# Optimization experiments

Measured on AMD Instinct MI355X. Metric: run time of the kernel, lower is better.

## Reference

```python
import jax, jax.numpy as jnp
import numpy as np

OUT_FEATURES = 4096
IN_FEATURES = 16384
NNZ = 2_000_000
BATCH = 128


def setup_inputs() -> dict:
    key = jax.random.key(0)
    k1, k2, k3, k4, k5 = jax.random.split(key, 5)
    inputs = jax.random.normal(k1, (BATCH, IN_FEATURES), dtype=jnp.float32)
    # learned sparse weight values and bias (uniform init like reset_parameters)
    bound = 1.0 / (IN_FEATURES ** 0.5)
    values = jax.random.uniform(k2, (NNZ,), minval=-bound, maxval=bound, dtype=jnp.float32)
    bias = jax.random.uniform(k3, (OUT_FEATURES,), minval=-bound, maxval=bound, dtype=jnp.float32)
    # fixed COO connectivity: rows -> out_features, cols -> in_features
    rows = jax.random.randint(k4, (NNZ,), 0, OUT_FEATURES, dtype=jnp.int32)
    cols = jax.random.randint(k5, (NNZ,), 0, IN_FEATURES, dtype=jnp.int32)
    return {"inputs": inputs, "values": values, "bias": bias, "rows": rows, "cols": cols}


def reference(inputs, values, bias, rows, cols):
    # out[b, r] = sum_{k: rows[k]==r} values[k] * inputs[b, cols[k]]  (+ bias[r])
    # Gather input columns per nnz entry, scale, then scatter-add into output rows.
    contrib = inputs[:, cols] * values            # [B, nnz]
    out = jax.ops.segment_sum(contrib.T, rows, num_segments=OUT_FEATURES).T  # [B, out_features]
    return out + bias
```

## Files before the change

### kernel.cpp

```cpp
#include <hip/hip_runtime.h>
#include <hip/hip_fp16.h>

#define NNZ    2000000
#define BATCH  128
#define IN_F   16384
#define OUT_F  4096
#define NCH    512
#define CHUNK  ((NNZ + NCH - 1) / NCH)
#define NBK    512
#define RPB    8
#define BK_CAP 4352
#define SP_CAP 2608

__global__ __launch_bounds__(512)
void k_bhist(const int* __restrict__ rows, int* __restrict__ bcntT) {
  __shared__ int h[NBK];
  const int t = threadIdx.x, c = blockIdx.x;
  h[t] = 0;
  __syncthreads();
  const int base = c * CHUNK;
  const int n = min(CHUNK, NNZ - base);
  for (int i = t; i < n; i += 512) atomicAdd(&h[rows[base + i] >> 3], 1);
  __syncthreads();
  bcntT[t * NCH + c] = h[t];
}

__global__ __launch_bounds__(256)
void k_cscan(int* __restrict__ bcntT, int* __restrict__ totals) {
  const int w = threadIdx.x >> 6, lane = threadIdx.x & 63;
  const int b = blockIdx.x * 4 + w;
  int4 u = ((const int4*)(bcntT + b * NCH))[lane * 2];
  int4 v = ((const int4*)(bcntT + b * NCH))[lane * 2 + 1];
  int p0 = 0, p1 = u.x, p2 = p1 + u.y, p3 = p2 + u.z, p4 = p3 + u.w;
  int p5 = p4 + v.x, p6 = p5 + v.y, p7 = p6 + v.z;
  int run = p7 + v.w;
  int x = run;
#pragma unroll
  for (int off = 1; off < 64; off <<= 1) { int y = __shfl_up(x, off); if (lane >= off) x += y; }
  const int e0 = x - run;
  int4 o0 = make_int4(e0 + p0, e0 + p1, e0 + p2, e0 + p3);
  int4 o1 = make_int4(e0 + p4, e0 + p5, e0 + p6, e0 + p7);
  ((int4*)(bcntT + b * NCH))[lane * 2] = o0;
  ((int4*)(bcntT + b * NCH))[lane * 2 + 1] = o1;
  if (lane == 63) totals[b] = x;
}

__global__ __launch_bounds__(64)
void k_sscan(const int* __restrict__ totals, int* __restrict__ bstart) {
  const int lane = threadIdx.x;
  int4 u = ((const int4*)totals)[lane * 2];
  int4 v = ((const int4*)totals)[lane * 2 + 1];
  int p0 = 0, p1 = u.x, p2 = p1 + u.y, p3 = p2 + u.z, p4 = p3 + u.w;
  int p5 = p4 + v.x, p6 = p5 + v.y, p7 = p6 + v.z;
  int run = p7 + v.w;
  int x = run;
#pragma unroll
  for (int off = 1; off < 64; off <<= 1) { int y = __shfl_up(x, off); if (lane >= off) x += y; }
  const int e0 = x - run;
  ((int4*)bstart)[lane * 2] = make_int4(e0 + p0, e0 + p1, e0 + p2, e0 + p3);
  ((int4*)bstart)[lane * 2 + 1] = make_int4(e0 + p4, e0 + p5, e0 + p6, e0 + p7);
  if (lane == 63) bstart[NBK] = x;
}

__global__ __launch_bounds__(512)
void k_bscatter(const int* __restrict__ rows, const int* __restrict__ cols,
                const float* __restrict__ vals, const int* __restrict__ bcntT,
                const int* __restrict__ bstart, int2* __restrict__ pairs1) {
  __shared__ int2 stage[CHUNK];
  __shared__ int h[NBK], lst[NBK], cnt[NBK], gb[NBK];
  const int t = threadIdx.x, c = blockIdx.x;
  h[t] = 0;
  __syncthreads();
  const int base = c * CHUNK;
  const int n = min(CHUNK, NNZ - base);
  for (int i = t; i < n; i += 512) atomicAdd(&h[rows[base + i] >> 3], 1);
  __syncthreads();
  if (t < 64) {
    const int l8 = t * 8;
    int v[8], pre[8], run = 0;
#pragma unroll
    for (int j = 0; j < 8; ++j) v[j] = h[l8 + j];
#pragma unroll
    for (int j = 0; j < 8; ++j) { pre[j] = run; run += v[j]; }
    int x = run;
#pragma unroll
    for (int off = 1; off < 64; off <<= 1) { int y = __shfl_up(x, off); if (t >= off) x += y; }
    const int e0 = x - run;
#pragma unroll
    for (int j = 0; j < 8; ++j) {
      const int b = l8 + j;
      const int lv = e0 + pre[j];
      lst[b] = lv; cnt[b] = lv;
      gb[b] = bstart[b] + bcntT[b * NCH + c] - lv;
    }
  }
  __syncthreads();
  for (int i = t; i < n; i += 512) {
    const int r = rows[base + i];
    const int pos = atomicAdd(&cnt[r >> 3], 1);
    stage[pos] = make_int2((r << 14) | cols[base + i], __float_as_int(vals[base + i]));
  }
  __syncthreads();
  for (int j = t; j < n; j += 512) {
    const int2 p = stage[j];
    pairs1[gb[p.x >> 17] + j] = p;
  }
}

__global__ __launch_bounds__(512)
void k_bsort(int2* __restrict__ pairs1, const int* __restrict__ bstart,
             int* __restrict__ row_start) {
  __shared__ int2 stage[BK_CAP];
  __shared__ int h[RPB], lst[RPB], cnt[RPB];
  const int t = threadIdx.x, b = blockIdx.x;
  const int s = bstart[b];
  const int nb = min(bstart[b + 1] - s, BK_CAP);
  if (t < RPB) h[t] = 0;
  __syncthreads();
  for (int i = t; i < nb; i += 512) {
    const int2 p = pairs1[s + i];
    stage[i] = p;
    atomicAdd(&h[(p.x >> 14) & 7], 1);
  }
  __syncthreads();
  if (t == 0) {
    int a = 0;
#pragma unroll
    for (int j = 0; j < RPB; ++j) { const int v = h[j]; lst[j] = a; cnt[j] = a; a += v; }
  }
  __syncthreads();
  if (t < RPB) row_start[b * RPB + t] = s + lst[t];
  if (b == 0 && t == RPB) row_start[OUT_F] = NNZ;
  for (int i = t; i < nb; i += 512) {
    const int2 p = stage[i];
    const int pos = atomicAdd(&cnt[(p.x >> 14) & 7], 1);
    pairs1[s + pos] = p;
  }
}

__global__ __launch_bounds__(256)
void k_transpose(const float* __restrict__ in, __half* __restrict__ inT) {
  __shared__ float tile[32][33];
  const int tx = threadIdx.x, ty = threadIdx.y;
  const int c0 = blockIdx.x * 32, b0 = blockIdx.y * 32;
#pragma unroll
  for (int j = 0; j < 32; j += 8)
    tile[ty + j][tx] = in[(b0 + ty + j) * IN_F + c0 + tx];
  __syncthreads();
#pragma unroll
  for (int j = 0; j < 32; j += 8)
    inT[(size_t)(c0 + ty + j) * BATCH + b0 + tx] = __float2half(tile[tx][ty + j]);
}

#define FMA8(V, X) do { \
    const __half2* hh = (const __half2*)&(X); \
    float2 f0 = __half22float2(hh[0]); \
    float2 f1 = __half22float2(hh[1]); \
    float2 f2 = __half22float2(hh[2]); \
    float2 f3 = __half22float2(hh[3]); \
    a0 = fmaf((V), f0.x, a0); a1 = fmaf((V), f0.y, a1); \
    a2 = fmaf((V), f1.x, a2); a3 = fmaf((V), f1.y, a3); \
    a4 = fmaf((V), f2.x, a4); a5 = fmaf((V), f2.y, a5); \
    a6 = fmaf((V), f3.x, a6); a7 = fmaf((V), f3.y, a7); \
  } while (0)

#define REFILL(SL, STEP) do { \
    const int idx = (STEP) * 8 + 2 * g; \
    const int2 p0 = lp[s + idx]; \
    const int2 p1 = lp[s + idx + 1]; \
    v##SL##0 = (idx < n) ? __int_as_float(p0.y) : 0.f; \
    v##SL##1 = (idx + 1 < n) ? __int_as_float(p1.y) : 0.f; \
    x##SL##0 = inT[(p0.x & 16383) * 16 + q]; \
    x##SL##1 = inT[(p1.x & 16383) * 16 + q]; \
  } while (0)

#define STAGE(SL, NEXTSTEP) do { \
    FMA8(v##SL##0, x##SL##0); \
    FMA8(v##SL##1, x##SL##1); \
    REFILL(SL, NEXTSTEP); \
  } while (0)

__global__ __launch_bounds__(256)
void k_spmm(const uint4* __restrict__ inT, const int2* __restrict__ pairs,
            const int* __restrict__ row_start, const float* __restrict__ bias,
            float* __restrict__ out) {
  __shared__ int2 lp[SP_CAP];
  const int t = threadIdx.x;
  const int wave = t >> 6, lane = t & 63;
  const int r0 = blockIdx.x * 4;
  const int bs = row_start[r0];
  const int nall = min(row_start[r0 + 4] - bs, SP_CAP);
  for (int i = t; i < nall; i += 256) lp[i] = pairs[bs + i];
  __syncthreads();

  const int r = r0 + wave;
  const int g = lane >> 4, q = lane & 15;
  const int s = row_start[r] - bs;
  const int n = row_start[r + 1] - bs - s;
  const int nsteps = (n + 7) >> 3;
  const int ns3 = ((nsteps + 2) / 3) * 3;

  float a0 = 0.f, a1 = 0.f, a2 = 0.f, a3 = 0.f, a4 = 0.f, a5 = 0.f, a6 = 0.f, a7 = 0.f;
  uint4 xA0, xA1, xB0, xB1, xC0, xC1;
  float vA0, vA1, vB0, vB1, vC0, vC1;

  REFILL(A, 0);
  REFILL(B, 1);
  REFILL(C, 2);
  for (int i = 0; i < ns3; i += 3) {
    STAGE(A, i + 3);
    STAGE(B, i + 4);
    STAGE(C, i + 5);
  }

  a0 += __shfl_xor(a0, 16); a0 += __shfl_xor(a0, 32);
  a1 += __shfl_xor(a1, 16); a1 += __shfl_xor(a1, 32);
  a2 += __shfl_xor(a2, 16); a2 += __shfl_xor(a2, 32);
  a3 += __shfl_xor(a3, 16); a3 += __shfl_xor(a3, 32);
  a4 += __shfl_xor(a4, 16); a4 += __shfl_xor(a4, 32);
  a5 += __shfl_xor(a5, 16); a5 += __shfl_xor(a5, 32);
  a6 += __shfl_xor(a6, 16); a6 += __shfl_xor(a6, 32);
  a7 += __shfl_xor(a7, 16); a7 += __shfl_xor(a7, 32);

  if (g == 0) {
    const float bs_ = bias[r];
    const int b0 = q * 8;
    out[(b0 + 0) * OUT_F + r] = a0 + bs_;
    out[(b0 + 1) * OUT_F + r] = a1 + bs_;
    out[(b0 + 2) * OUT_F + r] = a2 + bs_;
    out[(b0 + 3) * OUT_F + r] = a3 + bs_;
    out[(b0 + 4) * OUT_F + r] = a4 + bs_;
    out[(b0 + 5) * OUT_F + r] = a5 + bs_;
    out[(b0 + 6) * OUT_F + r] = a6 + bs_;
    out[(b0 + 7) * OUT_F + r] = a7 + bs_;
  }
}

extern "C" void kernel_launch(void* const* d_in, const int* in_sizes, int n_in,
                              void* d_out, int out_size, void* d_ws, size_t ws_size,
                              hipStream_t stream) {
  const float* inputs = (const float*)d_in[0];
  const float* values = (const float*)d_in[1];
  const float* bias   = (const float*)d_in[2];
  const int*   rows   = (const int*)d_in[3];
  const int*   cols   = (const int*)d_in[4];
  float* out = (float*)d_out;

  char* ws = (char*)d_ws;
  __half* inputT = (__half*)(ws);
  int2*   pairs1 = (int2*)(ws + 4194304);
  int*    bcntT  = (int*)(ws + 20194304);
  int*    totals = (int*)(ws + 21242880);
  int*    bstart = (int*)(ws + 21244928);
  int*    row_st = (int*)(ws + 21247040);

  k_bhist    <<<NCH,     512, 0, stream>>>(rows, bcntT);
  k_cscan    <<<NBK / 4, 256, 0, stream>>>(bcntT, totals);
  k_sscan    <<<1,        64, 0, stream>>>(totals, bstart);
  k_bscatter <<<NCH,     512, 0, stream>>>(rows, cols, values, bcntT, bstart, pairs1);
  k_bsort    <<<NBK,     512, 0, stream>>>(pairs1, bstart, row_st);
  k_transpose<<<dim3(IN_F / 32, BATCH / 32), dim3(32, 8), 0, stream>>>(inputs, inputT);
  k_spmm     <<<OUT_F / 4, 256, 0, stream>>>((const uint4*)inputT, pairs1, row_st, bias, out);
}
```

Baseline: 143.0 us.

## Replace histogram/scan pipeline with atomic bucket reservation and fuse row sort into SpMM

Drops the separate histogram, two scan kernels and bucket-sort kernel. Buckets now sit at fixed-capacity slots, and each chunk reserves its range with a global atomicAdd on a per-bucket cursor. The per-bucket row sort moves into the SpMM kernel, which now runs one 512-thread block per 8-row bucket and sorts in LDS before the gather-FMA loop. This removes several launches and a full global read/write pass over the pairs, but uses more LDS per block (two 4352-entry buffers). Bucket order within a slot becomes nondeterministic, which can change float summation order.

```diff
diff --git a/kernel.cpp b/kernel.cpp
--- a/kernel.cpp
+++ b/kernel.cpp
@@ -10,69 +10,18 @@
 #define NBK    512
 #define RPB    8
 #define BK_CAP 4352
-#define SP_CAP 2608
-
-__global__ __launch_bounds__(512)
-void k_bhist(const int* __restrict__ rows, int* __restrict__ bcntT) {
-  __shared__ int h[NBK];
-  const int t = threadIdx.x, c = blockIdx.x;
-  h[t] = 0;
-  __syncthreads();
-  const int base = c * CHUNK;
-  const int n = min(CHUNK, NNZ - base);
-  for (int i = t; i < n; i += 512) atomicAdd(&h[rows[base + i] >> 3], 1);
-  __syncthreads();
-  bcntT[t * NCH + c] = h[t];
-}
-
-__global__ __launch_bounds__(256)
-void k_cscan(int* __restrict__ bcntT, int* __restrict__ totals) {
-  const int w = threadIdx.x >> 6, lane = threadIdx.x & 63;
-  const int b = blockIdx.x * 4 + w;
-  int4 u = ((const int4*)(bcntT + b * NCH))[lane * 2];
-  int4 v = ((const int4*)(bcntT + b * NCH))[lane * 2 + 1];
-  int p0 = 0, p1 = u.x, p2 = p1 + u.y, p3 = p2 + u.z, p4 = p3 + u.w;
-  int p5 = p4 + v.x, p6 = p5 + v.y, p7 = p6 + v.z;
-  int run = p7 + v.w;
-  int x = run;
-#pragma unroll
-  for (int off = 1; off < 64; off <<= 1) { int y = __shfl_up(x, off); if (lane >= off) x += y; }
-  const int e0 = x - run;
-  int4 o0 = make_int4(e0 + p0, e0 + p1, e0 + p2, e0 + p3);
-  int4 o1 = make_int4(e0 + p4, e0 + p5, e0 + p6, e0 + p7);
-  ((int4*)(bcntT + b * NCH))[lane * 2] = o0;
-  ((int4*)(bcntT + b * NCH))[lane * 2 + 1] = o1;
-  if (lane == 63) totals[b] = x;
-}
-
-__global__ __launch_bounds__(64)
-void k_sscan(const int* __restrict__ totals, int* __restrict__ bstart) {
-  const int lane = threadIdx.x;
-  int4 u = ((const int4*)totals)[lane * 2];
-  int4 v = ((const int4*)totals)[lane * 2 + 1];
-  int p0 = 0, p1 = u.x, p2 = p1 + u.y, p3 = p2 + u.z, p4 = p3 + u.w;
-  int p5 = p4 + v.x, p6 = p5 + v.y, p7 = p6 + v.z;
-  int run = p7 + v.w;
-  int x = run;
-#pragma unroll
-  for (int off = 1; off < 64; off <<= 1) { int y = __shfl_up(x, off); if (lane >= off) x += y; }
-  const int e0 = x - run;
-  ((int4*)bstart)[lane * 2] = make_int4(e0 + p0, e0 + p1, e0 + p2, e0 + p3);
-  ((int4*)bstart)[lane * 2 + 1] = make_int4(e0 + p4, e0 + p5, e0 + p6, e0 + p7);
-  if (lane == 63) bstart[NBK] = x;
-}
 
 __global__ __launch_bounds__(512)
 void k_bscatter(const int* __restrict__ rows, const int* __restrict__ cols,
-                const float* __restrict__ vals, const int* __restrict__ bcntT,
-                const int* __restrict__ bstart, int2* __restrict__ pairs1) {
+                const float* __restrict__ vals, int* __restrict__ gcur,
+                int2* __restrict__ pairs1) {
   __shared__ int2 stage[CHUNK];
-  __shared__ int h[NBK], lst[NBK], cnt[NBK], gb[NBK];
+  __shared__ int h[NBK], cur[NBK], gb[NBK];
   const int t = threadIdx.x, c = blockIdx.x;
+  const int base = c * CHUNK;
+  const int n = min(CHUNK, NNZ - base);
   h[t] = 0;
   __syncthreads();
-  const int base = c * CHUNK;
-  const int n = min(CHUNK, NNZ - base);
   for (int i = t; i < n; i += 512) atomicAdd(&h[rows[base + i] >> 3], 1);
   __syncthreads();
   if (t < 64) {
@@ -89,52 +38,22 @@
 #pragma unroll
     for (int j = 0; j < 8; ++j) {
       const int b = l8 + j;
-      const int lv = e0 + pre[j];
-      lst[b] = lv; cnt[b] = lv;
-      gb[b] = bstart[b] + bcntT[b * NCH + c] - lv;
+      const int lex = e0 + pre[j];
+      cur[b] = lex;
+      const int gbase = atomicAdd(&gcur[b], v[j]);
+      gb[b] = b * BK_CAP + gbase - lex;
     }
   }
   __syncthreads();
   for (int i = t; i < n; i += 512) {
     const int r = rows[base + i];
-    const int pos = atomicAdd(&cnt[r >> 3], 1);
+    const int pos = atomicAdd(&cur[r >> 3], 1);
     stage[pos] = make_int2((r << 14) | cols[base + i], __float_as_int(vals[base + i]));
   }
   __syncthreads();
   for (int j = t; j < n; j += 512) {
     const int2 p = stage[j];
     pairs1[gb[p.x >> 17] + j] = p;
-  }
-}
-
-__global__ __launch_bounds__(512)
-void k_bsort(int2* __restrict__ pairs1, const int* __restrict__ bstart,
-             int* __restrict__ row_start) {
-  __shared__ int2 stage[BK_CAP];
-  __shared__ int h[RPB], lst[RPB], cnt[RPB];
-  const int t = threadIdx.x, b = blockIdx.x;
-  const int s = bstart[b];
-  const int nb = min(bstart[b + 1] - s, BK_CAP);
-  if (t < RPB) h[t] = 0;
-  __syncthreads();
-  for (int i = t; i < nb; i += 512) {
-    const int2 p = pairs1[s + i];
-    stage[i] = p;
-    atomicAdd(&h[(p.x >> 14) & 7], 1);
-  }
-  __syncthreads();
-  if (t == 0) {
-    int a = 0;
-#pragma unroll
-    for (int j = 0; j < RPB; ++j) { const int v = h[j]; lst[j] = a; cnt[j] = a; a += v; }
-  }
-  __syncthreads();
-  if (t < RPB) row_start[b * RPB + t] = s + lst[t];
-  if (b == 0 && t == RPB) row_start[OUT_F] = NNZ;
-  for (int i = t; i < nb; i += 512) {
-    const int2 p = stage[i];
-    const int pos = atomicAdd(&cnt[(p.x >> 14) & 7], 1);
-    pairs1[s + pos] = p;
   }
 }
 
@@ -166,10 +85,12 @@
 
 #define REFILL(SL, STEP) do { \
     const int idx = (STEP) * 8 + 2 * g; \
-    const int2 p0 = lp[s + idx]; \
-    const int2 p1 = lp[s + idx + 1]; \
-    v##SL##0 = (idx < n) ? __int_as_float(p0.y) : 0.f; \
-    v##SL##1 = (idx + 1 < n) ? __int_as_float(p1.y) : 0.f; \
+    const int i0_ = (idx < nr) ? (s + idx) : 0; \
+    const int i1_ = (idx + 1 < nr) ? (s + idx + 1) : 0; \
+    const int2 p0 = sorted[i0_]; \
+    const int2 p1 = sorted[i1_]; \
+    v##SL##0 = (idx < nr) ? __int_as_float(p0.y) : 0.f; \
+    v##SL##1 = (idx + 1 < nr) ? __int_as_float(p1.y) : 0.f; \
     x##SL##0 = inT[(p0.x & 16383) * 16 + q]; \
     x##SL##1 = inT[(p1.x & 16383) * 16 + q]; \
   } while (0)
@@ -180,24 +101,44 @@
     REFILL(SL, NEXTSTEP); \
   } while (0)
 
-__global__ __launch_bounds__(256)
-void k_spmm(const uint4* __restrict__ inT, const int2* __restrict__ pairs,
-            const int* __restrict__ row_start, const float* __restrict__ bias,
+__global__ __launch_bounds__(512)
+void k_spmm(const uint4* __restrict__ inT, const int2* __restrict__ pairs1,
+            const int* __restrict__ gcur, const float* __restrict__ bias,
             float* __restrict__ out) {
-  __shared__ int2 lp[SP_CAP];
-  const int t = threadIdx.x;
+  __shared__ int2 stagep[BK_CAP];
+  __shared__ int2 sorted[BK_CAP];
+  __shared__ int h[RPB], lst[RPB + 1], cur8[RPB];
+  const int t = threadIdx.x, b = blockIdx.x;
   const int wave = t >> 6, lane = t & 63;
-  const int r0 = blockIdx.x * 4;
-  const int bs = row_start[r0];
-  const int nall = min(row_start[r0 + 4] - bs, SP_CAP);
-  for (int i = t; i < nall; i += 256) lp[i] = pairs[bs + i];
+  const int n = min(gcur[b], BK_CAP);
+  const int base = b * BK_CAP;
+  if (t < RPB) h[t] = 0;
+  __syncthreads();
+  for (int i = t; i < n; i += 512) {
+    const int2 p = pairs1[base + i];
+    stagep[i] = p;
+    atomicAdd(&h[(p.x >> 14) & 7], 1);
+  }
+  __syncthreads();
+  if (t == 0) {
+    int run = 0;
+#pragma unroll
+    for (int j = 0; j < RPB; ++j) { lst[j] = run; cur8[j] = run; run += h[j]; }
+    lst[RPB] = run;
+  }
+  __syncthreads();
+  for (int i = t; i < n; i += 512) {
+    const int2 p = stagep[i];
+    const int pos = atomicAdd(&cur8[(p.x >> 14) & 7], 1);
+    sorted[pos] = p;
+  }
   __syncthreads();
 
-  const int r = r0 + wave;
+  const int r = b * RPB + wave;
   const int g = lane >> 4, q = lane & 15;
-  const int s = row_start[r] - bs;
-  const int n = row_start[r + 1] - bs - s;
-  const int nsteps = (n + 7) >> 3;
+  const int s = lst[wave];
+  const int nr = lst[wave + 1] - s;
+  const int nsteps = (nr + 7) >> 3;
   const int ns3 = ((nsteps + 2) / 3) * 3;
 
   float a0 = 0.f, a1 = 0.f, a2 = 0.f, a3 = 0.f, a4 = 0.f, a5 = 0.f, a6 = 0.f, a7 = 0.f;
@@ -249,16 +190,10 @@
   char* ws = (char*)d_ws;
   __half* inputT = (__half*)(ws);
   int2*   pairs1 = (int2*)(ws + 4194304);
-  int*    bcntT  = (int*)(ws + 20194304);
-  int*    totals = (int*)(ws + 21242880);
-  int*    bstart = (int*)(ws + 21244928);
-  int*    row_st = (int*)(ws + 21247040);
+  int*    gcur   = (int*)(ws + 22020096);
 
-  k_bhist    <<<NCH,     512, 0, stream>>>(rows, bcntT);
-  k_cscan    <<<NBK / 4, 256, 0, stream>>>(bcntT, totals);
-  k_sscan    <<<1,        64, 0, stream>>>(totals, bstart);
-  k_bscatter <<<NCH,     512, 0, stream>>>(rows, cols, values, bcntT, bstart, pairs1);
-  k_bsort    <<<NBK,     512, 0, stream>>>(pairs1, bstart, row_st);
+  hipMemsetAsync(gcur, 0, NBK * sizeof(int), stream);
+  k_bscatter <<<NCH, 512, 0, stream>>>(rows, cols, values, gcur, pairs1);
   k_transpose<<<dim3(IN_F / 32, BATCH / 32), dim3(32, 8), 0, stream>>>(inputs, inputT);
-  k_spmm     <<<OUT_F / 4, 256, 0, stream>>>((const uint4*)inputT, pairs1, row_st, bias, out);
+  k_spmm     <<<NBK, 512, 0, stream>>>((const uint4*)inputT, pairs1, gcur, bias, out);
 }
```

After: 203.7 us. 1.42x slower.

## Fuse per-bucket row sort into SpMM kernel using wave ballot ranking

Applied to the files above, without the earlier changes.

Removes the separate k_bsort kernel and its global round-trip of the pairs array and row_start. Each SpMM block now handles a whole 8-row bucket with 512 threads. It loads the bucket once, does a stable counting sort by row in shared memory using ballot masks and mbcnt ranks, then runs the per-row gather-FMA loop from the sorted shared copy. This saves a kernel launch and one read-write pass over 16 MB. In exchange, block count drops to 512 with larger blocks and more shared memory per block, which may reduce occupancy for the gather phase.

```diff
diff --git a/kernel.cpp b/kernel.cpp
--- a/kernel.cpp
+++ b/kernel.cpp
@@ -10,7 +10,11 @@
 #define NBK    512
 #define RPB    8
 #define BK_CAP 4352
-#define SP_CAP 2608
+
+__device__ inline int mbcnt64(unsigned long long m) {
+  return __builtin_amdgcn_mbcnt_hi((unsigned)(m >> 32),
+         __builtin_amdgcn_mbcnt_lo((unsigned)m, 0));
+}
 
 __global__ __launch_bounds__(512)
 void k_bhist(const int* __restrict__ rows, int* __restrict__ bcntT) {
@@ -38,10 +42,8 @@
 #pragma unroll
   for (int off = 1; off < 64; off <<= 1) { int y = __shfl_up(x, off); if (lane >= off) x += y; }
   const int e0 = x - run;
-  int4 o0 = make_int4(e0 + p0, e0 + p1, e0 + p2, e0 + p3);
-  int4 o1 = make_int4(e0 + p4, e0 + p5, e0 + p6, e0 + p7);
-  ((int4*)(bcntT + b * NCH))[lane * 2] = o0;
-  ((int4*)(bcntT + b * NCH))[lane * 2 + 1] = o1;
+  ((int4*)(bcntT + b * NCH))[lane * 2] = make_int4(e0 + p0, e0 + p1, e0 + p2, e0 + p3);
+  ((int4*)(bcntT + b * NCH))[lane * 2 + 1] = make_int4(e0 + p4, e0 + p5, e0 + p6, e0 + p7);
   if (lane == 63) totals[b] = x;
 }
 
@@ -67,12 +69,12 @@
                 const float* __restrict__ vals, const int* __restrict__ bcntT,
                 const int* __restrict__ bstart, int2* __restrict__ pairs1) {
   __shared__ int2 stage[CHUNK];
-  __shared__ int h[NBK], lst[NBK], cnt[NBK], gb[NBK];
+  __shared__ int h[NBK], cur[NBK], gb[NBK];
   const int t = threadIdx.x, c = blockIdx.x;
-  h[t] = 0;
-  __syncthreads();
   const int base = c * CHUNK;
   const int n = min(CHUNK, NNZ - base);
+  h[t] = 0;
+  __syncthreads();
   for (int i = t; i < n; i += 512) atomicAdd(&h[rows[base + i] >> 3], 1);
   __syncthreads();
   if (t < 64) {
@@ -89,52 +91,21 @@
 #pragma unroll
     for (int j = 0; j < 8; ++j) {
       const int b = l8 + j;
-      const int lv = e0 + pre[j];
-      lst[b] = lv; cnt[b] = lv;
-      gb[b] = bstart[b] + bcntT[b * NCH + c] - lv;
+      const int lex = e0 + pre[j];
+      cur[b] = lex;
+      gb[b] = bstart[b] + bcntT[b * NCH + c] - lex;
     }
   }
   __syncthreads();
   for (int i = t; i < n; i += 512) {
     const int r = rows[base + i];
-    const int pos = atomicAdd(&cnt[r >> 3], 1);
+    const int pos = atomicAdd(&cur[r >> 3], 1);
     stage[pos] = make_int2((r << 14) | cols[base + i], __float_as_int(vals[base + i]));
   }
   __syncthreads();
   for (int j = t; j < n; j += 512) {
     const int2 p = stage[j];
     pairs1[gb[p.x >> 17] + j] = p;
-  }
-}
-
-__global__ __launch_bounds__(512)
-void k_bsort(int2* __restrict__ pairs1, const int* __restrict__ bstart,
-             int* __restrict__ row_start) {
-  __shared__ int2 stage[BK_CAP];
-  __shared__ int h[RPB], lst[RPB], cnt[RPB];
-  const int t = threadIdx.x, b = blockIdx.x;
-  const int s = bstart[b];
-  const int nb = min(bstart[b + 1] - s, BK_CAP);
-  if (t < RPB) h[t] = 0;
-  __syncthreads();
-  for (int i = t; i < nb; i += 512) {
-    const int2 p = pairs1[s + i];
-    stage[i] = p;
-    atomicAdd(&h[(p.x >> 14) & 7], 1);
-  }
-  __syncthreads();
-  if (t == 0) {
-    int a = 0;
-#pragma unroll
-    for (int j = 0; j < RPB; ++j) { const int v = h[j]; lst[j] = a; cnt[j] = a; a += v; }
-  }
-  __syncthreads();
-  if (t < RPB) row_start[b * RPB + t] = s + lst[t];
-  if (b == 0 && t == RPB) row_start[OUT_F] = NNZ;
-  for (int i = t; i < nb; i += 512) {
-    const int2 p = stage[i];
-    const int pos = atomicAdd(&cnt[(p.x >> 14) & 7], 1);
-    pairs1[s + pos] = p;
   }
 }
 
@@ -166,10 +137,12 @@
 
 #define REFILL(SL, STEP) do { \
     const int idx = (STEP) * 8 + 2 * g; \
-    const int2 p0 = lp[s + idx]; \
-    const int2 p1 = lp[s + idx + 1]; \
-    v##SL##0 = (idx < n) ? __int_as_float(p0.y) : 0.f; \
-    v##SL##1 = (idx + 1 < n) ? __int_as_float(p1.y) : 0.f; \
+    const int i0_ = (idx < nr) ? (s + idx) : 0; \
+    const int i1_ = (idx + 1 < nr) ? (s + idx + 1) : 0; \
+    const int2 p0 = sorted[i0_]; \
+    const int2 p1 = sorted[i1_]; \
+    v##SL##0 = (idx < nr) ? __int_as_float(p0.y) : 0.f; \
+    v##SL##1 = (idx + 1 < nr) ? __int_as_float(p1.y) : 0.f; \
     x##SL##0 = inT[(p0.x & 16383) * 16 + q]; \
     x##SL##1 = inT[(p1.x & 16383) * 16 + q]; \
   } while (0)
@@ -180,24 +153,74 @@
     REFILL(SL, NEXTSTEP); \
   } while (0)
 
-__global__ __launch_bounds__(256)
-void k_spmm(const uint4* __restrict__ inT, const int2* __restrict__ pairs,
-            const int* __restrict__ row_start, const float* __restrict__ bias,
+__global__ __launch_bounds__(512)
+void k_spmm(const uint4* __restrict__ inT, const int2* __restrict__ pairs1,
+            const int* __restrict__ bstart, const float* __restrict__ bias,
             float* __restrict__ out) {
-  __shared__ int2 lp[SP_CAP];
-  const int t = threadIdx.x;
-  const int wave = t >> 6, lane = t & 63;
-  const int r0 = blockIdx.x * 4;
-  const int bs = row_start[r0];
-  const int nall = min(row_start[r0 + 4] - bs, SP_CAP);
-  for (int i = t; i < nall; i += 256) lp[i] = pairs[bs + i];
-  __syncthreads();
-
-  const int r = r0 + wave;
+  __shared__ int2 sorted[BK_CAP];
+  __shared__ int  wrun[64];
+  __shared__ unsigned long long wmask[64];
+  __shared__ int  wcnt[64];
+  __shared__ int  lst[RPB + 1];
+  const int t = threadIdx.x, b = blockIdx.x;
+  const int w = t >> 6, lane = t & 63;
+  const int s0 = bstart[b];
+  const int n = min(bstart[b + 1] - s0, BK_CAP);
+  const int nrnd = (n + 511) & ~511;
+
+  int cnt = 0;
+  for (int i = w * 64 + lane; i < nrnd; i += 512) {
+    const bool valid = i < n;
+    const int key = valid ? pairs1[s0 + i].x : 0;
+    const int r8 = valid ? ((key >> 14) & 7) : 8;
+    unsigned long long m[8];
+#pragma unroll
+    for (int r = 0; r < 8; ++r) m[r] = __ballot(r8 == r);
+    if (lane < 8) cnt += __popcll(m[lane]);
+  }
+  if (lane < 8) wcnt[w * 8 + lane] = cnt;
+  __syncthreads();
+
+  if (w == 0) {
+    const int v = wcnt[lane];
+    int x = v;
+#pragma unroll
+    for (int off = 8; off < 64; off <<= 1) { int y = __shfl_up(x, off); if (lane >= off) x += y; }
+    const int excl_w = x - v;
+    int lstr = 0;
+#pragma unroll
+    for (int rr = 0; rr < 8; ++rr) {
+      const int tr = __shfl(x, 56 + rr);
+      if ((lane & 7) > rr) lstr += tr;
+    }
+    wrun[lane] = lstr + excl_w;
+    if (lane < 8) lst[lane] = lstr;
+    if (lane == 0) lst[8] = n;
+  }
+  __syncthreads();
+
+  for (int i = w * 64 + lane; i < nrnd; i += 512) {
+    const bool valid = i < n;
+    const int2 p = valid ? pairs1[s0 + i] : make_int2(0, 0);
+    const int r8 = valid ? ((p.x >> 14) & 7) : 8;
+    unsigned long long m[8];
+#pragma unroll
+    for (int r = 0; r < 8; ++r) m[r] = __ballot(r8 == r);
+    if (lane < 8) wmask[w * 8 + lane] = m[lane];
+    if (valid) {
+      const unsigned long long mm = wmask[w * 8 + r8];
+      const int rank = wrun[w * 8 + r8] + mbcnt64(mm);
+      sorted[rank] = p;
+    }
+    if (lane < 8) wrun[w * 8 + lane] += __popcll(m[lane]);
+  }
+  __syncthreads();
+
+  const int r = b * RPB + w;
   const int g = lane >> 4, q = lane & 15;
-  const int s = row_start[r] - bs;
-  const int n = row_start[r + 1] - bs - s;
-  const int nsteps = (n + 7) >> 3;
+  const int s = lst[w];
+  const int nr = lst[w + 1] - s;
+  const int nsteps = (nr + 7) >> 3;
   const int ns3 = ((nsteps + 2) / 3) * 3;
 
   float a0 = 0.f, a1 = 0.f, a2 = 0.f, a3 = 0.f, a4 = 0.f, a5 = 0.f, a6 = 0.f, a7 = 0.f;
@@ -252,13 +275,11 @@
   int*    bcntT  = (int*)(ws + 20194304);
   int*    totals = (int*)(ws + 21242880);
   int*    bstart = (int*)(ws + 21244928);
-  int*    row_st = (int*)(ws + 21247040);
 
   k_bhist    <<<NCH,     512, 0, stream>>>(rows, bcntT);
   k_cscan    <<<NBK / 4, 256, 0, stream>>>(bcntT, totals);
   k_sscan    <<<1,        64, 0, stream>>>(totals, bstart);
   k_bscatter <<<NCH,     512, 0, stream>>>(rows, cols, values, bcntT, bstart, pairs1);
-  k_bsort    <<<NBK,     512, 0, stream>>>(pairs1, bstart, row_st);
   k_transpose<<<dim3(IN_F / 32, BATCH / 32), dim3(32, 8), 0, stream>>>(inputs, inputT);
-  k_spmm     <<<OUT_F / 4, 256, 0, stream>>>((const uint4*)inputT, pairs1, row_st, bias, out);
-}
+  k_spmm     <<<NBK,     512, 0, stream>>>((const uint4*)inputT, pairs1, bstart, bias, out);
+}
```

Measured after the change: 139.6 us. 1.02x faster.
